# Kernel tuning notes

Measured on AMD Instinct MI355X. Metric: run time of the kernel, lower is better.

## Reference

```python
import jax, jax.numpy as jnp
import numpy as np
from jax import lax

CONF_BIT = 8        # mantissa bits for block-floating-point
CONF_GROUP_SIZE = 36  # elements sharing one exponent


def bfp_quantize(x, bits=CONF_BIT, group_size=CONF_GROUP_SIZE):
    """Group-wise block-floating-point quantization (make_groups_tensor).
    Consecutive groups of `group_size` elements of the flattened tensor share
    the exponent of the group's max magnitude; mantissas are rounded to `bits` bits."""
    shape = x.shape
    flat = x.reshape(-1)
    n = flat.shape[0]
    pad = (-n) % group_size
    flat = jnp.pad(flat, (0, pad))
    g = flat.reshape(-1, group_size)
    max_abs = jnp.max(jnp.abs(g), axis=1, keepdims=True)
    # shared exponent = floor(log2(max|x|)); guard zero groups
    exp = jnp.floor(jnp.log2(jnp.where(max_abs > 0, max_abs, 1.0)))
    step = jnp.exp2(exp - (bits - 1))  # quantization step per group
    qmax = 2 ** (bits - 1) - 1
    q = jnp.clip(jnp.round(g / step), -(qmax + 1), qmax) * step
    q = jnp.where(max_abs > 0, q, 0.0)
    return q.reshape(-1)[:n].reshape(shape)


def setup_inputs() -> dict:
    key = jax.random.key(0)
    k1, k2, k3 = jax.random.split(key, 3)
    B, Cin, Cout, H, W, K = 32, 128, 128, 112, 112, 3
    x = jax.random.normal(k1, (B, Cin, H, W), dtype=jnp.float32)
    fan_in = Cin * K * K
    weight = jax.random.normal(k2, (Cout, Cin, K, K), dtype=jnp.float32) / np.sqrt(fan_in)
    bound = 1.0 / np.sqrt(fan_in)
    bias = jax.random.uniform(k3, (Cout,), dtype=jnp.float32, minval=-bound, maxval=bound)
    return {"x": x, "weight": weight, "bias": bias}


def reference(x, weight, bias):
    # BFP-quantize input and weight, then plain conv2d (stride=1, padding=1)
    xq = bfp_quantize(x)
    wq = bfp_quantize(weight)
    out = lax.conv_general_dilated(
        xq, wq,
        window_strides=(1, 1),
        padding=((1, 1), (1, 1)),
        dimension_numbers=("NCHW", "OIHW", "NCHW"),
    )
    return out + bias[None, :, None, None]
```

## Files before the change

kernel.cpp:

```cpp
#include <hip/hip_runtime.h>

typedef __attribute__((ext_vector_type(8))) short short8;
typedef __attribute__((ext_vector_type(4))) float f32x4;

#define NB     32
#define NC     128
#define HW     112
#define PLANE  12544
#define XTOT   51380224
#define NGX    1427229
#define PADW   114
#define PADPLANE 12996
#define XPAD_BYTES 106463232ULL
#define WG_OFF     XPAD_BYTES
#define SE_OFF     (XPAD_BYTES + 294912ULL)

__device__ __forceinline__ void gld_lds16(const void* g, void* l) {
  __builtin_amdgcn_global_load_lds(
      (__attribute__((address_space(1))) unsigned int*)g,
      (__attribute__((address_space(3))) unsigned int*)l, 16, 0, 0);
}

__device__ __forceinline__ float qmax4(float4 v, float m) {
  m = fmaxf(m, fabsf(v.x)); m = fmaxf(m, fabsf(v.y));
  m = fmaxf(m, fabsf(v.z)); m = fmaxf(m, fabsf(v.w));
  return m;
}

__device__ __forceinline__ int bfp_exp(float m) {
  int e = 0;
  if (m > 0.f) {
    e = (int)((__float_as_uint(m) >> 23) & 255) - 127;
    if (e < -100) e = -100;
  }
  return e;
}

__device__ __forceinline__ unsigned short bfp_q(float v, float inv, float st) {
  float qq = fminf(fmaxf(rintf(v * inv), -128.f), 127.f) * st;
  return (unsigned short)(__float_as_uint(qq) >> 16);
}

__global__ __launch_bounds__(256) void quant_step_x(const float* __restrict__ x,
                                                    signed char* __restrict__ se) {
  int g = blockIdx.x * 256 + threadIdx.x;
  if (g >= NGX) return;
  int base = g * 36;
  float m = 0.f;
  if (base + 36 <= XTOT) {
    const float4* p4 = (const float4*)(x + base);
#pragma unroll
    for (int j = 0; j < 9; ++j) m = qmax4(p4[j], m);
  } else {
    for (int i = base; i < XTOT; ++i) m = fmaxf(m, fabsf(x[i]));
  }
  se[g] = (signed char)bfp_exp(m);
}

__global__ __launch_bounds__(64) void quant_w_kernel(const float* __restrict__ w,
                                                     unsigned short* __restrict__ wg) {
  int g = blockIdx.x * 64 + threadIdx.x;
  if (g >= 4096) return;
  const float4* p4 = (const float4*)(w + g * 36);
  float4 v[9];
  float m = 0.f;
#pragma unroll
  for (int j = 0; j < 9; ++j) { v[j] = p4[j]; m = qmax4(v[j], m); }
  int e = bfp_exp(m);
  float inv = __uint_as_float((unsigned)(134 - e) << 23);
  float st  = __uint_as_float((unsigned)(120 + e) << 23);
#pragma unroll
  for (int j = 0; j < 9; ++j) {
    float tmp[4] = {v[j].x, v[j].y, v[j].z, v[j].w};
#pragma unroll
    for (int k = 0; k < 4; ++k) {
      int i = j * 4 + k;
      int f = g * 36 + i;
      int co = f / 1152;
      int rem = f % 1152;
      int ci = rem / 9;
      int rs = rem % 9;
      int stp = rs * 4 + (ci >> 5);
      wg[(stp * 128 + co) * 32 + (ci & 31)] = bfp_q(tmp[i & 3] * 0.f + tmp[k], inv, st);
    }
  }
}

__global__ __launch_bounds__(256) void border_zero(unsigned short* __restrict__ xpad) {
  int tid = blockIdx.x * 256 + threadIdx.x;
  if (tid >= NB * 452 * 16) return;
  int b = tid / (452 * 16);
  int r = tid % (452 * 16);
  int pos = r >> 4, cc = r & 15;
  int hp, wp;
  if (pos < 114)      { hp = 0;             wp = pos; }
  else if (pos < 228) { hp = 113;           wp = pos - 114; }
  else if (pos < 340) { hp = pos - 228 + 1; wp = 0; }
  else                { hp = pos - 340 + 1; wp = 113; }
  float4 z = make_float4(0.f, 0.f, 0.f, 0.f);
  *(float4*)&xpad[((size_t)((b * 114 + hp) * 114 + wp)) * 128 + cc * 8] = z;
}

__global__ __launch_bounds__(256) void quant_pad_x(const float* __restrict__ x,
                                                   const signed char* __restrict__ se,
                                                   unsigned short* __restrict__ xpad) {
  __shared__ unsigned short tile[32 * 128];
  int b = blockIdx.y;
  int p0 = blockIdx.x * 32;
  int t = threadIdx.x;
  int pq  = (t & 7) * 4;
  int ci0 = (t >> 3) * 4;
  unsigned short q[4][4];
#pragma unroll
  for (int i = 0; i < 4; ++i) {
    int ci = ci0 + i;
    int f = (b * 128 + ci) * PLANE + p0 + pq;
    float4 v = *(const float4*)(x + f);
    float vv[4] = {v.x, v.y, v.z, v.w};
#pragma unroll
    for (int j = 0; j < 4; ++j) {
      int e = se[(f + j) / 36];
      float inv = __uint_as_float((unsigned)(134 - e) << 23);
      float st  = __uint_as_float((unsigned)(120 + e) << 23);
      q[i][j] = bfp_q(vv[j], inv, st);
    }
  }
#pragma unroll
  for (int j = 0; j < 4; ++j)
    *(ushort4*)&tile[(pq + j) * 128 + ci0] = make_ushort4(q[0][j], q[1][j], q[2][j], q[3][j]);
  __syncthreads();
  int pl = t >> 3;
  int cc = t & 7;
  int p = p0 + pl;
  int h = p / 112, w = p % 112;
  float4 v0 = *(const float4*)&tile[pl * 128 + cc * 16];
  float4 v1 = *(const float4*)&tile[pl * 128 + cc * 16 + 8];
  size_t dst = ((size_t)((b * 114 + h + 1) * 114 + (w + 1))) * 128 + cc * 16;
  *(float4*)&xpad[dst]     = v0;
  *(float4*)&xpad[dst + 8] = v1;
}

__global__ __launch_bounds__(256) void conv_mfma(const unsigned short* __restrict__ xpad,
                                                 const unsigned short* __restrict__ wg,
                                                 const float* __restrict__ bias,
                                                 float* __restrict__ out) {
  __shared__ unsigned short smem[8192];
  char* smb = (char*)smem;
  const int t = threadIdx.x;
  const int lane = t & 63, wv = t >> 6;
  const int lane15 = lane & 15, quad = lane >> 4;
  const int wm = wv >> 1, wn = wv & 1;
  const int b = blockIdx.y;
  const int p0 = blockIdx.x * 128;

  int a_src[2], b_src[2];
#pragma unroll
  for (int i = 0; i < 2; ++i) {
    int idx = t + i * 256;
    int row = idx >> 2;
    int c = idx & 3;
    int sw = (row >> 1) & 3;
    a_src[i] = row * 32 + (c ^ sw) * 8;
    int p = p0 + row;
    int h = p / 112, ww = p % 112;
    b_src[i] = ((b * 114 + h) * 114 + ww) * 128 + (c ^ sw) * 8;
  }

  int a_off[4], b_off[4];
#pragma unroll
  for (int f = 0; f < 4; ++f) {
    int row = wm * 64 + f * 16 + lane15;
    a_off[f] = row * 64 + ((quad ^ ((row >> 1) & 3)) * 16);
    int prow = wn * 64 + f * 16 + lane15;
    b_off[f] = 8192 + prow * 64 + ((quad ^ ((prow >> 1) & 3)) * 16);
  }

  f32x4 acc[4][4];
  f32x4 zero = {0.f, 0.f, 0.f, 0.f};
#pragma unroll
  for (int i = 0; i < 4; ++i)
#pragma unroll
    for (int j = 0; j < 4; ++j) acc[i][j] = zero;

  for (int step = 0; step < 36; ++step) {
    int rs = step >> 2, cib = step & 3;
    int r = rs / 3, s = rs % 3;
    int aofs = step * 4096;
    int bofs = (r * 114 + s) * 128 + cib * 32;
    __syncthreads();
#pragma unroll
    for (int i = 0; i < 2; ++i) {
      gld_lds16(wg + aofs + a_src[i],   smb + wv * 1024 + i * 4096);
      gld_lds16(xpad + b_src[i] + bofs, smb + 8192 + wv * 1024 + i * 4096);
    }
    __syncthreads();
    short8 af[4], bf[4];
#pragma unroll
    for (int f = 0; f < 4; ++f) af[f] = *(const short8*)(smb + a_off[f]);
#pragma unroll
    for (int f = 0; f < 4; ++f) bf[f] = *(const short8*)(smb + b_off[f]);
#pragma unroll
    for (int i = 0; i < 4; ++i)
#pragma unroll
      for (int j = 0; j < 4; ++j)
        acc[i][j] = __builtin_amdgcn_mfma_f32_16x16x32_bf16(af[i], bf[j], acc[i][j], 0, 0, 0);
  }

#pragma unroll
  for (int i = 0; i < 4; ++i)
#pragma unroll
    for (int j = 0; j < 4; ++j) {
      int p = p0 + wn * 64 + j * 16 + lane15;
#pragma unroll
      for (int rr = 0; rr < 4; ++rr) {
        int co = wm * 64 + i * 16 + quad * 4 + rr;
        out[(b * 128 + co) * PLANE + p] = acc[i][j][rr] + bias[co];
      }
    }
}

extern "C" void kernel_launch(void* const* d_in, const int* in_sizes, int n_in,
                              void* d_out, int out_size, void* d_ws, size_t ws_size,
                              hipStream_t stream) {
  const float* x    = (const float*)d_in[0];
  const float* w    = (const float*)d_in[1];
  const float* bias = (const float*)d_in[2];
  float* out = (float*)d_out;
  char* ws = (char*)d_ws;
  unsigned short* xpad = (unsigned short*)ws;
  unsigned short* wg   = (unsigned short*)(ws + WG_OFF);
  signed char*    se   = (signed char*)(ws + SE_OFF);

  quant_step_x<<<(NGX + 255) / 256, 256, 0, stream>>>(x, se);
  quant_w_kernel<<<64, 64, 0, stream>>>(w, wg);
  border_zero<<<904, 256, 0, stream>>>(xpad);
  quant_pad_x<<<dim3(392, 32), 256, 0, stream>>>(x, se, xpad);
  conv_mfma<<<dim3(98, 32), 256, 0, stream>>>(xpad, wg, bias, out);
}
```

Before: 556.2 us.

## Double-buffer conv LDS stages, fuse border zeroing, stage exponent scan through LDS

The conv kernel now double-buffers its LDS tiles, so the next step's global-to-LDS loads are issued before the MFMAs on the current buffer, with one barrier per step instead of two. The border-zero kernel is folded into quant_pad_x, removing one launch. quant_step_x stages its input through LDS with coalesced float4 loads instead of strided per-thread reads. The transpose tile gets a padded stride to reduce LDS bank conflicts. The cost is doubled LDS per conv block, which may lower occupancy.

```diff
diff --git a/kernel.cpp b/kernel.cpp
--- a/kernel.cpp
+++ b/kernel.cpp
@@ -43,17 +43,25 @@
 
 __global__ __launch_bounds__(256) void quant_step_x(const float* __restrict__ x,
                                                     signed char* __restrict__ se) {
-  int g = blockIdx.x * 256 + threadIdx.x;
+  __shared__ float lds[9216];
+  const int t = threadIdx.x;
+  const int base = blockIdx.x * 9216;
+  const float4* src = (const float4*)(x + base);
+  const int rem4 = (XTOT - base) >> 2;
+#pragma unroll
+  for (int j = 0; j < 9; ++j) {
+    int idx = j * 256 + t;
+    float4 v = make_float4(0.f, 0.f, 0.f, 0.f);
+    if (idx < rem4) v = src[idx];
+    ((float4*)lds)[idx] = v;
+  }
+  __syncthreads();
+  int g = blockIdx.x * 256 + t;
   if (g >= NGX) return;
-  int base = g * 36;
+  const float4* p4 = (const float4*)(lds + t * 36);
   float m = 0.f;
-  if (base + 36 <= XTOT) {
-    const float4* p4 = (const float4*)(x + base);
-#pragma unroll
-    for (int j = 0; j < 9; ++j) m = qmax4(p4[j], m);
-  } else {
-    for (int i = base; i < XTOT; ++i) m = fmaxf(m, fabsf(x[i]));
-  }
+#pragma unroll
+  for (int j = 0; j < 9; ++j) m = qmax4(p4[j], m);
   se[g] = (signed char)bfp_exp(m);
 }
 
@@ -81,33 +89,34 @@
       int ci = rem / 9;
       int rs = rem % 9;
       int stp = rs * 4 + (ci >> 5);
-      wg[(stp * 128 + co) * 32 + (ci & 31)] = bfp_q(tmp[i & 3] * 0.f + tmp[k], inv, st);
-    }
-  }
-}
-
-__global__ __launch_bounds__(256) void border_zero(unsigned short* __restrict__ xpad) {
-  int tid = blockIdx.x * 256 + threadIdx.x;
-  if (tid >= NB * 452 * 16) return;
-  int b = tid / (452 * 16);
-  int r = tid % (452 * 16);
-  int pos = r >> 4, cc = r & 15;
-  int hp, wp;
-  if (pos < 114)      { hp = 0;             wp = pos; }
-  else if (pos < 228) { hp = 113;           wp = pos - 114; }
-  else if (pos < 340) { hp = pos - 228 + 1; wp = 0; }
-  else                { hp = pos - 340 + 1; wp = 113; }
-  float4 z = make_float4(0.f, 0.f, 0.f, 0.f);
-  *(float4*)&xpad[((size_t)((b * 114 + hp) * 114 + wp)) * 128 + cc * 8] = z;
-}
-
+      wg[(stp * 128 + co) * 32 + (ci & 31)] = bfp_q(tmp[k], inv, st);
+    }
+  }
+}
+
+#define TSTR 136
 __global__ __launch_bounds__(256) void quant_pad_x(const float* __restrict__ x,
                                                    const signed char* __restrict__ se,
                                                    unsigned short* __restrict__ xpad) {
-  __shared__ unsigned short tile[32 * 128];
+  __shared__ unsigned short tile[32 * TSTR];
   int b = blockIdx.y;
   int p0 = blockIdx.x * 32;
   int t = threadIdx.x;
+
+  int hid = (blockIdx.y * 392 + blockIdx.x) * 256 + t;
+  if (hid < NB * 452 * 16) {
+    int hb = hid / (452 * 16);
+    int r = hid % (452 * 16);
+    int pos = r >> 4, cc = r & 15;
+    int hp, wp;
+    if (pos < 114)      { hp = 0;             wp = pos; }
+    else if (pos < 228) { hp = 113;           wp = pos - 114; }
+    else if (pos < 340) { hp = pos - 228 + 1; wp = 0; }
+    else                { hp = pos - 340 + 1; wp = 113; }
+    float4 z = make_float4(0.f, 0.f, 0.f, 0.f);
+    *(float4*)&xpad[((size_t)((hb * 114 + hp) * 114 + wp)) * 128 + cc * 8] = z;
+  }
+
   int pq  = (t & 7) * 4;
   int ci0 = (t >> 3) * 4;
   unsigned short q[4][4];
@@ -127,14 +136,14 @@
   }
 #pragma unroll
   for (int j = 0; j < 4; ++j)
-    *(ushort4*)&tile[(pq + j) * 128 + ci0] = make_ushort4(q[0][j], q[1][j], q[2][j], q[3][j]);
+    *(ushort4*)&tile[(pq + j) * TSTR + ci0] = make_ushort4(q[0][j], q[1][j], q[2][j], q[3][j]);
   __syncthreads();
   int pl = t >> 3;
   int cc = t & 7;
   int p = p0 + pl;
   int h = p / 112, w = p % 112;
-  float4 v0 = *(const float4*)&tile[pl * 128 + cc * 16];
-  float4 v1 = *(const float4*)&tile[pl * 128 + cc * 16 + 8];
+  float4 v0 = *(const float4*)&tile[pl * TSTR + cc * 16];
+  float4 v1 = *(const float4*)&tile[pl * TSTR + cc * 16 + 8];
   size_t dst = ((size_t)((b * 114 + h + 1) * 114 + (w + 1))) * 128 + cc * 16;
   *(float4*)&xpad[dst]     = v0;
   *(float4*)&xpad[dst + 8] = v1;
@@ -144,7 +153,7 @@
                                                  const unsigned short* __restrict__ wg,
                                                  const float* __restrict__ bias,
                                                  float* __restrict__ out) {
-  __shared__ unsigned short smem[8192];
+  __shared__ unsigned short smem[16384];
   char* smb = (char*)smem;
   const int t = threadIdx.x;
   const int lane = t & 63, wv = t >> 6;
@@ -182,28 +191,44 @@
 #pragma unroll
     for (int j = 0; j < 4; ++j) acc[i][j] = zero;
 
-  for (int step = 0; step < 36; ++step) {
+  auto stage = [&](int step, char* dst) {
     int rs = step >> 2, cib = step & 3;
-    int r = rs / 3, s = rs % 3;
+    int r = (rs * 11) >> 5;
+    int s = rs - r * 3;
     int aofs = step * 4096;
     int bofs = (r * 114 + s) * 128 + cib * 32;
-    __syncthreads();
 #pragma unroll
     for (int i = 0; i < 2; ++i) {
-      gld_lds16(wg + aofs + a_src[i],   smb + wv * 1024 + i * 4096);
-      gld_lds16(xpad + b_src[i] + bofs, smb + 8192 + wv * 1024 + i * 4096);
-    }
-    __syncthreads();
+      gld_lds16(wg + aofs + a_src[i],   dst + wv * 1024 + i * 4096);
+      gld_lds16(xpad + b_src[i] + bofs, dst + 8192 + wv * 1024 + i * 4096);
+    }
+  };
+
+  auto compute = [&](const char* sb) {
     short8 af[4], bf[4];
 #pragma unroll
-    for (int f = 0; f < 4; ++f) af[f] = *(const short8*)(smb + a_off[f]);
-#pragma unroll
-    for (int f = 0; f < 4; ++f) bf[f] = *(const short8*)(smb + b_off[f]);
+    for (int f = 0; f < 4; ++f) af[f] = *(const short8*)(sb + a_off[f]);
+#pragma unroll
+    for (int f = 0; f < 4; ++f) bf[f] = *(const short8*)(sb + b_off[f]);
 #pragma unroll
     for (int i = 0; i < 4; ++i)
 #pragma unroll
       for (int j = 0; j < 4; ++j)
         acc[i][j] = __builtin_amdgcn_mfma_f32_16x16x32_bf16(af[i], bf[j], acc[i][j], 0, 0, 0);
+  };
+
+  char* B0 = smb;
+  char* B1 = smb + 16384;
+
+  stage(0, B0);
+  __syncthreads();
+  for (int it = 0; it < 18; ++it) {
+    stage(2 * it + 1, B1);
+    compute(B0);
+    __syncthreads();
+    if (it < 17) stage(2 * it + 2, B0);
+    compute(B1);
+    __syncthreads();
   }
 
 #pragma unroll
@@ -233,7 +258,6 @@
 
   quant_step_x<<<(NGX + 255) / 256, 256, 0, stream>>>(x, se);
   quant_w_kernel<<<64, 64, 0, stream>>>(w, wg);
-  border_zero<<<904, 256, 0, stream>>>(xpad);
   quant_pad_x<<<dim3(392, 32), 256, 0, stream>>>(x, se, xpad);
   conv_mfma<<<dim3(98, 32), 256, 0, stream>>>(xpad, wg, bias, out);
 }
```

After: 553.1 us. About the same (-0.6%).
